# Optimization experiments

Measured on AMD Instinct MI355X. Metric: run time of the kernel, lower is better.

The kernel has to match this reference:

```python
import jax, jax.numpy as jnp
import numpy as np

FUSE_W = 0.3
TEMP = 0.1
TOPK = 8
EPS = 1e-8


def _l2n(x, eps=EPS):
    return x / (jnp.linalg.norm(x, axis=-1, keepdims=True) + eps)


def setup_inputs() -> dict:
    key = jax.random.key(0)
    ks = jax.random.split(key, 6)
    B, Dk, Dv, N = 4096, 512, 512, 65536
    return {
        "q": jax.random.normal(ks[0], (B, Dk), jnp.float32),
        "spike_key": (jax.random.uniform(ks[1], (B, Dk)) > 0.5).astype(jnp.float32),
        "mem_keys": jax.random.normal(ks[2], (N, Dk), jnp.float32),
        "mem_values": jax.random.normal(ks[3], (N, Dv), jnp.float32),
        "W": jax.random.normal(ks[4], (Dk, Dk), jnp.float32) / np.sqrt(Dk).astype(np.float32),
        "b": jnp.zeros((Dk,), jnp.float32),
    }


def reference(q, spike_key, mem_keys, mem_values, W, b):
    # MemoryCube.query with spike fusion; memory fully filled (N = capacity).
    qn = _l2n(q)                                    # (B, Dk)
    enc = spike_key @ W.T + b                       # spike_encoder Linear
    qn = _l2n((1.0 - FUSE_W) * qn + FUSE_W * enc)   # _fuse_key
    keys_n = _l2n(mem_keys)                         # (N, Dk)
    sims = qn @ keys_n.T                            # (B, N) cosine sims
    top_vals, top_idx = jax.lax.top_k(sims, TOPK)   # (B, K)
    attn = jax.nn.softmax(top_vals / TEMP, axis=-1)
    vals = mem_values[top_idx]                      # (B, K, Dv) gather
    out = jnp.einsum('bk,bkd->bd', attn, vals)      # weighted combine
    # entropy-based confidence
    p = jnp.clip(attn, EPS, None)
    H = -(p * jnp.log(p)).sum(axis=-1)
    H_max = jnp.log(jnp.float32(TOPK))
    conf = (1.0 - H / (H_max + EPS)).mean()
    return out, conf, top_idx, attn
```

## Files before the change

kernel.cpp:

```cpp
#include <hip/hip_runtime.h>
#include <stdint.h>
#include <math.h>

typedef unsigned short u16;
typedef __attribute__((ext_vector_type(2))) float floatx2;
typedef __attribute__((ext_vector_type(4))) float floatx4;
typedef __attribute__((ext_vector_type(4))) unsigned int uintx4;
typedef __attribute__((ext_vector_type(8))) __bf16 bf16x8;

#define B_ROWS 4096
#define DK 512
#define NKEYS 65536
#define NCHUNK 32
#define CHUNK (NKEYS / NCHUNK)
#define SLOTS 32
#define CAND_PER_ROW (NCHUNK * SLOTS)
#define THRESH 0.135f

#define CONF_OFF 2097152
#define IDX_OFF  2097153
#define ATTN_OFF (IDX_OFF + B_ROWS * 8)

__device__ __forceinline__ u16 f2bf(float x) {
    union { float f; unsigned int u; } v; v.f = x;
    unsigned int r = v.u + 0x7fffu + ((v.u >> 16) & 1u);
    return (u16)(r >> 16);
}

__device__ __forceinline__ void gload_lds16(const u16* g, u16* l) {
    __builtin_amdgcn_global_load_lds(
        (const __attribute__((address_space(1))) unsigned int*)g,
        (__attribute__((address_space(3))) unsigned int*)l,
        16, 0, 0);
}

__device__ __forceinline__ float np_block128_sq(const float* a) {
#pragma clang fp contract(off)
    float r[8];
    floatx4 p0 = *(const floatx4*)&a[0];
    floatx4 p1 = *(const floatx4*)&a[4];
    r[0] = p0.x * p0.x; r[1] = p0.y * p0.y; r[2] = p0.z * p0.z; r[3] = p0.w * p0.w;
    r[4] = p1.x * p1.x; r[5] = p1.y * p1.y; r[6] = p1.z * p1.z; r[7] = p1.w * p1.w;
    for (int i = 8; i < 128; i += 8) {
        floatx4 q0 = *(const floatx4*)&a[i];
        floatx4 q1 = *(const floatx4*)&a[i + 4];
        r[0] += q0.x * q0.x; r[1] += q0.y * q0.y;
        r[2] += q0.z * q0.z; r[3] += q0.w * q0.w;
        r[4] += q1.x * q1.x; r[5] += q1.y * q1.y;
        r[6] += q1.z * q1.z; r[7] += q1.w * q1.w;
    }
    return ((r[0] + r[1]) + (r[2] + r[3])) + ((r[4] + r[5]) + (r[6] + r[7]));
}

__device__ __forceinline__ float np_sum512_sq(const float* a) {
#pragma clang fp contract(off)
    float b0 = np_block128_sq(a);
    float b1 = np_block128_sq(a + 128);
    float b2 = np_block128_sq(a + 256);
    float b3 = np_block128_sq(a + 384);
    return (b0 + b1) + (b2 + b3);
}

__device__ __forceinline__ float sqrt_f32_cr(float s) {
    return (float)sqrt((double)s);
}
__device__ __forceinline__ float div_f32_cr(float a, float b) {
    return (float)((double)a / (double)b);
}

__global__ __launch_bounds__(256) void transpose_w(const float* __restrict__ w,
                                                   float* __restrict__ wt) {
    int j = blockIdx.x, t = threadIdx.x;
    float a = w[(size_t)j * DK + t];
    float b = w[(size_t)j * DK + t + 256];
    wt[(size_t)t * DK + j] = a;
    wt[(size_t)(t + 256) * DK + j] = b;
}

__global__ __launch_bounds__(256) void prep_keys(float* __restrict__ mk,
                                                 u16* __restrict__ kbf) {
    const int row = blockIdx.x * 256 + threadIdx.x;
    float* kp = mk + (size_t)row * DK;
    float s = np_sum512_sq(kp);
    float nrm = sqrt_f32_cr(s) + 1e-8f;
    for (int i = 0; i < DK; i += 8) {
        floatx4 p0 = *(const floatx4*)&kp[i];
        floatx4 p1 = *(const floatx4*)&kp[i + 4];
        floatx4 n0, n1;
        n0.x = div_f32_cr(p0.x, nrm); n0.y = div_f32_cr(p0.y, nrm);
        n0.z = div_f32_cr(p0.z, nrm); n0.w = div_f32_cr(p0.w, nrm);
        n1.x = div_f32_cr(p1.x, nrm); n1.y = div_f32_cr(p1.y, nrm);
        n1.z = div_f32_cr(p1.z, nrm); n1.w = div_f32_cr(p1.w, nrm);
        union { uintx4 v; u16 u[8]; } pk;
        pk.u[0] = f2bf(n0.x); pk.u[1] = f2bf(n0.y);
        pk.u[2] = f2bf(n0.z); pk.u[3] = f2bf(n0.w);
        pk.u[4] = f2bf(n1.x); pk.u[5] = f2bf(n1.y);
        pk.u[6] = f2bf(n1.z); pk.u[7] = f2bf(n1.w);
        *(floatx4*)&kp[i] = n0;
        *(floatx4*)&kp[i + 4] = n1;
        *(uintx4*)&kbf[(size_t)row * DK + i] = pk.v;
    }
}

__global__ __launch_bounds__(256) void fuse_q(const float* __restrict__ q,
                                              const float* __restrict__ spike,
                                              const float* __restrict__ wt,
                                              const float* __restrict__ bvec,
                                              float* __restrict__ qn2f,
                                              u16* __restrict__ qbf) {
    __shared__ __align__(16) float s_sp[DK];
    __shared__ __align__(16) float s_q[DK];
    __shared__ __align__(16) float s_y[DK];
    __shared__ float s_nq;
    __shared__ float s_ny;
    const int t = threadIdx.x, b = blockIdx.x;
    s_sp[t] = spike[(size_t)b * DK + t];
    s_sp[t + 256] = spike[(size_t)b * DK + t + 256];
    s_q[t] = q[(size_t)b * DK + t];
    s_q[t + 256] = q[(size_t)b * DK + t + 256];
    __syncthreads();

    const int c0 = 2 * t;
    float a0 = 0.f, a1 = 0.f;
    for (int i = 0; i < DK; i += 16) {
        float sv[16]; floatx2 wv[16];
#pragma unroll
        for (int u = 0; u < 16; ++u) {
            sv[u] = s_sp[i + u];
            wv[u] = *(const floatx2*)&wt[(size_t)(i + u) * DK + c0];
        }
#pragma unroll
        for (int u = 0; u < 16; ++u) {
            a0 = fmaf(sv[u], wv[u].x, a0);
            a1 = fmaf(sv[u], wv[u].y, a1);
        }
    }

    if (t == 0) s_nq = sqrt_f32_cr(np_sum512_sq(s_q)) + 1e-8f;
    __syncthreads();
    float nq = s_nq;
    float qn0 = div_f32_cr(s_q[c0], nq);
    float qn1 = div_f32_cr(s_q[c0 + 1], nq);
    float e0 = a0 + bvec[c0];
    float e1 = a1 + bvec[c0 + 1];
    float y0, y1;
    {
#pragma clang fp contract(off)
        float u0 = 0.7f * qn0; float v0 = 0.3f * e0; y0 = u0 + v0;
        float u1 = 0.7f * qn1; float v1 = 0.3f * e1; y1 = u1 + v1;
    }
    s_y[c0] = y0; s_y[c0 + 1] = y1;
    __syncthreads();
    if (t == 0) s_ny = sqrt_f32_cr(np_sum512_sq(s_y)) + 1e-8f;
    __syncthreads();
    float ny = s_ny;
    float f0 = div_f32_cr(y0, ny);
    float f1 = div_f32_cr(y1, ny);
    *(floatx2*)&qn2f[(size_t)b * DK + c0] = (floatx2){f0, f1};
    union { unsigned int u; u16 h[2]; } pk;
    pk.h[0] = f2bf(f0); pk.h[1] = f2bf(f1);
    *(unsigned int*)&qbf[(size_t)b * DK + c0] = pk.u;
}

__global__ __launch_bounds__(256, 4) void cand_gemm(const u16* __restrict__ qbf,
                                                    const u16* __restrict__ kbf,
                                                    int* __restrict__ cidx,
                                                    int* __restrict__ gcnt) {
    __shared__ u16 ldsA[128 * 64];
    __shared__ u16 ldsB[128 * 64];
    const int t = threadIdx.x;
    const int lane = t & 63;
    const int wave = t >> 6;
    const int qbase = blockIdx.x * 128;
    const int chunk = blockIdx.y;
    const int r0 = 64 * (wave >> 1), c0 = 64 * (wave & 1);
    const int quad = lane >> 4, m16 = lane & 15;

    const int srow = lane >> 3;
    const int scol = ((lane & 7) ^ srow) << 3;

    const u16* aBase = qbf + (size_t)(qbase + wave * 32 + srow) * DK + scol;

    floatx4 acc[4][4];

    for (int iter = 0; iter < CHUNK / 128; ++iter) {
        const int nbase = chunk * CHUNK + iter * 128;
        const u16* bBase = kbf + (size_t)(nbase + wave * 32 + srow) * DK + scol;
#pragma unroll
        for (int i = 0; i < 4; ++i)
#pragma unroll
            for (int j = 0; j < 4; ++j) acc[i][j] = (floatx4){0.f, 0.f, 0.f, 0.f};

        for (int ks = 0; ks < DK; ks += 64) {
            __syncthreads();
#pragma unroll
            for (int c = 0; c < 4; ++c) {
                const int m = wave * 4 + c;
                gload_lds16(aBase + (size_t)c * 8 * DK + ks, &ldsA[m * 512]);
                gload_lds16(bBase + (size_t)c * 8 * DK + ks, &ldsB[m * 512]);
            }
            __syncthreads();
#pragma unroll
            for (int h = 0; h < 2; ++h) {
                const int cb = ((h * 4 + quad) ^ (m16 & 7)) << 4;
                bf16x8 afr[4], bfr[4];
#pragma unroll
                for (int i = 0; i < 4; ++i)
                    afr[i] = __builtin_bit_cast(bf16x8,
                        *(const uintx4*)((const char*)ldsA + (r0 + 16 * i + m16) * 128 + cb));
#pragma unroll
                for (int j = 0; j < 4; ++j)
                    bfr[j] = __builtin_bit_cast(bf16x8,
                        *(const uintx4*)((const char*)ldsB + (c0 + 16 * j + m16) * 128 + cb));
#pragma unroll
                for (int i = 0; i < 4; ++i)
#pragma unroll
                    for (int j = 0; j < 4; ++j)
                        acc[i][j] = __builtin_amdgcn_mfma_f32_16x16x32_bf16(
                            afr[i], bfr[j], acc[i][j], 0, 0, 0);
            }
        }
#pragma unroll
        for (int i = 0; i < 4; ++i)
#pragma unroll
            for (int j = 0; j < 4; ++j) {
                int col = nbase + c0 + 16 * j + m16;
#pragma unroll
                for (int r = 0; r < 4; ++r) {
                    float v = acc[i][j][r];
                    if (v > THRESH) {
                        int grow = qbase + r0 + 16 * i + quad * 4 + r;
                        int slot = atomicAdd(&gcnt[grow * NCHUNK + chunk], 1);
                        if (slot < SLOTS)
                            cidx[(size_t)grow * CAND_PER_ROW + chunk * SLOTS + slot] = col;
                    }
                }
            }
    }
}

__global__ __launch_bounds__(256) void finalize_rows(const int* __restrict__ cidx,
                                                     const int* __restrict__ gcnt,
                                                     const float* __restrict__ qn2f,
                                                     const float* __restrict__ keys_n,
                                                     const float* __restrict__ mem_values,
                                                     float* __restrict__ out,
                                                     double* __restrict__ confp) {
    __shared__ __align__(16) float s_q[DK];
    __shared__ int s_cnt[NCHUNK];
    __shared__ int s_kin[CAND_PER_ROW];
    __shared__ float s_dv[CAND_PER_ROW];
    __shared__ int s_di[CAND_PER_ROW];
    __shared__ int s_n;
    __shared__ float s_lv[64][8];
    __shared__ int s_li[64][8];
    __shared__ float s_tv[8];
    __shared__ int s_ti[8];
    __shared__ double s_attn[8];

    const int b = blockIdx.x, t = threadIdx.x, lane = t & 63, wave = t >> 6;
    s_q[t] = qn2f[(size_t)b * DK + t];
    s_q[t + 256] = qn2f[(size_t)b * DK + t + 256];
    if (t == 0) s_n = 0;
    if (t < NCHUNK) {
        int c = gcnt[b * NCHUNK + t];
        s_cnt[t] = c < SLOTS ? c : SLOTS;
    }
    __syncthreads();

    for (int s = t; s < CAND_PER_ROW; s += 256) {
        int ch = s >> 5, sl = s & 31;
        if (sl < s_cnt[ch]) {
            int pos = atomicAdd(&s_n, 1);
            s_kin[pos] = cidx[(size_t)b * CAND_PER_ROW + s];
        }
    }
    __syncthreads();
    const int n = s_n;

    for (int p = t; p < n; p += 256) {
        int ki = s_kin[p];
        const float* kp = keys_n + (size_t)ki * DK;
        float acc = 0.f;
        for (int i = 0; i < DK; i += 4) {
            floatx4 kv = *(const floatx4*)&kp[i];
            acc = fmaf(s_q[i + 0], kv.x, acc);
            acc = fmaf(s_q[i + 1], kv.y, acc);
            acc = fmaf(s_q[i + 2], kv.z, acc);
            acc = fmaf(s_q[i + 3], kv.w, acc);
        }
        s_dv[p] = acc;
        s_di[p] = ki;
    }
    __syncthreads();

    if (wave == 0) {
        float lv[8]; int li[8];
#pragma unroll
        for (int k = 0; k < 8; ++k) { lv[k] = -1e30f; li[k] = 0x7fffffff; }
        for (int p = lane; p < n; p += 64) {
            float v = s_dv[p];
            int ki = s_di[p];
            if (v > lv[7] || (v == lv[7] && ki < li[7])) {
                lv[7] = v; li[7] = ki;
#pragma unroll
                for (int k = 7; k > 0; --k) {
                    bool sw = (lv[k] > lv[k - 1]) ||
                              (lv[k] == lv[k - 1] && li[k] < li[k - 1]);
                    if (sw) {
                        float tv = lv[k]; lv[k] = lv[k - 1]; lv[k - 1] = tv;
                        int ti = li[k]; li[k] = li[k - 1]; li[k - 1] = ti;
                    }
                }
            }
        }
#pragma unroll
        for (int k = 0; k < 8; ++k) { s_lv[lane][k] = lv[k]; s_li[lane][k] = li[k]; }
    }
    __syncthreads();

    if (t == 0) {
        int head[64];
#pragma unroll
        for (int l = 0; l < 64; ++l) head[l] = 0;
        for (int k = 0; k < 8; ++k) {
            float bv = -2e30f; int bi = 0x7fffffff; int bl = 0;
            for (int l = 0; l < 64; ++l) {
                int h = head[l];
                float v = s_lv[l][h];
                int ki = s_li[l][h];
                if (v > bv || (v == bv && ki < bi)) { bv = v; bi = ki; bl = l; }
            }
            head[bl]++;
            s_tv[k] = bv;
            s_ti[k] = (bi == 0x7fffffff) ? 0 : bi;
        }
        double mx = (double)s_tv[0];
        double e[8], sum = 0.0;
#pragma unroll
        for (int k = 0; k < 8; ++k) {
            e[k] = exp(((double)s_tv[k] - mx) / 0.1);
            sum += e[k];
        }
        double H = 0.0;
#pragma unroll
        for (int k = 0; k < 8; ++k) {
            double pa = e[k] / sum;
            s_attn[k] = pa;
            double pc = pa < 1e-8 ? 1e-8 : pa;
            H -= pc * log(pc);
        }
        confp[b] = 1.0 - H / (log(8.0) + 1e-8);
    }
    __syncthreads();

    if (t < 8) {
        out[IDX_OFF + (size_t)b * 8 + t] = (float)s_ti[t];
        out[ATTN_OFF + (size_t)b * 8 + t] = (float)s_attn[t];
    }
    for (int c = t; c < DK; c += 256) {
        double a = 0.0;
#pragma unroll
        for (int k = 0; k < 8; ++k)
            a += s_attn[k] * (double)mem_values[(size_t)s_ti[k] * DK + c];
        out[(size_t)b * DK + c] = (float)a;
    }
}

__global__ __launch_bounds__(256) void conf_reduce(const double* __restrict__ confp,
                                                   float* __restrict__ out) {
    __shared__ double red[256];
    int t = threadIdx.x;
    double s = 0.0;
    for (int i = t; i < B_ROWS; i += 256) s += confp[i];
    red[t] = s;
    __syncthreads();
    for (int k = 128; k > 0; k >>= 1) {
        if (t < k) red[t] += red[t + k];
        __syncthreads();
    }
    if (t == 0) out[CONF_OFF] = (float)(red[0] / 4096.0);
}

extern "C" void kernel_launch(void* const* d_in, const int* in_sizes, int n_in,
                              void* d_out, int out_size, void* d_ws, size_t ws_size,
                              hipStream_t stream) {
    const float* q     = (const float*)d_in[0];
    const float* spike = (const float*)d_in[1];
    float*       mk    = (float*)d_in[2];
    const float* mv    = (const float*)d_in[3];
    const float* w     = (const float*)d_in[4];
    const float* bvec  = (const float*)d_in[5];
    float* out = (float*)d_out;
    char* ws = (char*)d_ws;

    u16*    qbf   = (u16*)   (ws);
    u16*    kbf   = (u16*)   (ws + (4ull  << 20));
    float*  qn2f  = (float*) (ws + (68ull << 20));
    int*    cidx  = (int*)   (ws + (76ull << 20));
    float*  wt    = (float*) (ws + (92ull << 20));
    int*    gcnt  = (int*)   (ws + (93ull << 20));
    double* confp = (double*)(ws + (94ull << 20));

    hipMemsetAsync(gcnt, 0, (size_t)B_ROWS * NCHUNK * sizeof(int), stream);

    transpose_w<<<512, 256, 0, stream>>>(w, wt);
    prep_keys<<<NKEYS / 256, 256, 0, stream>>>(mk, kbf);
    fuse_q<<<B_ROWS, 256, 0, stream>>>(q, spike, wt, bvec, qn2f, qbf);
    cand_gemm<<<dim3(B_ROWS / 128, NCHUNK), 256, 0, stream>>>(qbf, kbf, cidx, gcnt);
    finalize_rows<<<B_ROWS, 256, 0, stream>>>(cidx, gcnt, qn2f, mk, mv, out, confp);
    conf_reduce<<<1, 256, 0, stream>>>(confp, out);
}
```

Baseline: 1.563 ms.

## Double-buffer key tiles in LDS and load query fragments directly from global

The candidate GEMM now keeps two LDS buffers for the key tile and prefetches the next k-step's key slice while the MFMAs run on the current one. This replaces the two barriers per step with a single one. The query tile is no longer staged in LDS; each wave reads its A fragments directly from global memory (cached in L1/L2) at every k-step. This removes A-tile LDS traffic and one sync per step, but it adds repeated global loads for A and puts their latency directly in front of the MFMAs.

```diff
diff --git a/kernel.cpp b/kernel.cpp
--- a/kernel.cpp
+++ b/kernel.cpp
@@ -166,8 +166,7 @@
                                                     const u16* __restrict__ kbf,
                                                     int* __restrict__ cidx,
                                                     int* __restrict__ gcnt) {
-    __shared__ u16 ldsA[128 * 64];
-    __shared__ u16 ldsB[128 * 64];
+    __shared__ u16 ldsB[2][128 * 64];
     const int t = threadIdx.x;
     const int lane = t & 63;
     const int wave = t >> 6;
@@ -179,63 +178,85 @@
     const int srow = lane >> 3;
     const int scol = ((lane & 7) ^ srow) << 3;
 
-    const u16* aBase = qbf + (size_t)(qbase + wave * 32 + srow) * DK + scol;
+    const u16* aRow = qbf + (size_t)(qbase + r0 + m16) * DK + quad * 8;
 
     floatx4 acc[4][4];
 
-    for (int iter = 0; iter < CHUNK / 128; ++iter) {
+    {
+        const u16* bB = kbf + (size_t)(chunk * CHUNK + wave * 32 + srow) * DK + scol;
+#pragma unroll
+        for (int c = 0; c < 4; ++c)
+            gload_lds16(bB + (size_t)c * 8 * DK, &ldsB[0][(wave * 4 + c) * 512]);
+    }
+    __syncthreads();
+
+    int cur = 0;
+    for (int s = 0; s < 128; ++s) {
+        const int iter = s >> 3;
+        const int ks = (s & 7) << 6;
         const int nbase = chunk * CHUNK + iter * 128;
-        const u16* bBase = kbf + (size_t)(nbase + wave * 32 + srow) * DK + scol;
-#pragma unroll
-        for (int i = 0; i < 4; ++i)
-#pragma unroll
-            for (int j = 0; j < 4; ++j) acc[i][j] = (floatx4){0.f, 0.f, 0.f, 0.f};
-
-        for (int ks = 0; ks < DK; ks += 64) {
-            __syncthreads();
-#pragma unroll
-            for (int c = 0; c < 4; ++c) {
-                const int m = wave * 4 + c;
-                gload_lds16(aBase + (size_t)c * 8 * DK + ks, &ldsA[m * 512]);
-                gload_lds16(bBase + (size_t)c * 8 * DK + ks, &ldsB[m * 512]);
-            }
-            __syncthreads();
-#pragma unroll
-            for (int h = 0; h < 2; ++h) {
-                const int cb = ((h * 4 + quad) ^ (m16 & 7)) << 4;
-                bf16x8 afr[4], bfr[4];
-#pragma unroll
-                for (int i = 0; i < 4; ++i)
-                    afr[i] = __builtin_bit_cast(bf16x8,
-                        *(const uintx4*)((const char*)ldsA + (r0 + 16 * i + m16) * 128 + cb));
+
+        if ((s & 7) == 0) {
+#pragma unroll
+            for (int i = 0; i < 4; ++i)
+#pragma unroll
+                for (int j = 0; j < 4; ++j) acc[i][j] = (floatx4){0.f, 0.f, 0.f, 0.f};
+        }
+
+        bf16x8 afr[2][4];
+#pragma unroll
+        for (int h = 0; h < 2; ++h)
+#pragma unroll
+            for (int i = 0; i < 4; ++i)
+                afr[h][i] = __builtin_bit_cast(bf16x8,
+                    *(const uintx4*)(aRow + (size_t)i * 16 * DK + ks + h * 32));
+
+        if (s < 127) {
+            const int s2 = s + 1;
+            const int nb2 = chunk * CHUNK + (s2 >> 3) * 128;
+            const int ks2 = (s2 & 7) << 6;
+            const u16* bB = kbf + (size_t)(nb2 + wave * 32 + srow) * DK + ks2 + scol;
+#pragma unroll
+            for (int c = 0; c < 4; ++c)
+                gload_lds16(bB + (size_t)c * 8 * DK, &ldsB[cur ^ 1][(wave * 4 + c) * 512]);
+        }
+
+#pragma unroll
+        for (int h = 0; h < 2; ++h) {
+            const int cb = ((h * 4 + quad) ^ (m16 & 7)) << 4;
+            bf16x8 bfr[4];
+#pragma unroll
+            for (int j = 0; j < 4; ++j)
+                bfr[j] = __builtin_bit_cast(bf16x8,
+                    *(const uintx4*)((const char*)&ldsB[cur][0] + (c0 + 16 * j + m16) * 128 + cb));
+#pragma unroll
+            for (int i = 0; i < 4; ++i)
 #pragma unroll
                 for (int j = 0; j < 4; ++j)
-                    bfr[j] = __builtin_bit_cast(bf16x8,
-                        *(const uintx4*)((const char*)ldsB + (c0 + 16 * j + m16) * 128 + cb));
-#pragma unroll
-                for (int i = 0; i < 4; ++i)
-#pragma unroll
-                    for (int j = 0; j < 4; ++j)
-                        acc[i][j] = __builtin_amdgcn_mfma_f32_16x16x32_bf16(
-                            afr[i], bfr[j], acc[i][j], 0, 0, 0);
-            }
-        }
-#pragma unroll
-        for (int i = 0; i < 4; ++i)
-#pragma unroll
-            for (int j = 0; j < 4; ++j) {
-                int col = nbase + c0 + 16 * j + m16;
-#pragma unroll
-                for (int r = 0; r < 4; ++r) {
-                    float v = acc[i][j][r];
-                    if (v > THRESH) {
-                        int grow = qbase + r0 + 16 * i + quad * 4 + r;
-                        int slot = atomicAdd(&gcnt[grow * NCHUNK + chunk], 1);
-                        if (slot < SLOTS)
-                            cidx[(size_t)grow * CAND_PER_ROW + chunk * SLOTS + slot] = col;
+                    acc[i][j] = __builtin_amdgcn_mfma_f32_16x16x32_bf16(
+                        afr[h][i], bfr[j], acc[i][j], 0, 0, 0);
+        }
+
+        if ((s & 7) == 7) {
+#pragma unroll
+            for (int i = 0; i < 4; ++i)
+#pragma unroll
+                for (int j = 0; j < 4; ++j) {
+                    int col = nbase + c0 + 16 * j + m16;
+#pragma unroll
+                    for (int r = 0; r < 4; ++r) {
+                        float v = acc[i][j][r];
+                        if (v > THRESH) {
+                            int grow = qbase + r0 + 16 * i + quad * 4 + r;
+                            int slot = atomicAdd(&gcnt[grow * NCHUNK + chunk], 1);
+                            if (slot < SLOTS)
+                                cidx[(size_t)grow * CAND_PER_ROW + chunk * SLOTS + slot] = col;
+                        }
                     }
                 }
-            }
+        }
+        __syncthreads();
+        cur ^= 1;
     }
 }
 
```

New measurement: 1.624 ms. 3.9% more time.
